# Performance work log

Hardware: AMD Instinct MI355X
Metric: run time of the kernel (lower is better)

The kernel has to match this reference:

```python
import jax, jax.numpy as jnp
import numpy as np

GAMMA = 2.0       # focal gamma (alpha=4.0 is unused in the original forward)
NC_LOOP = 20      # original loops cls in range(n_classes + 1) = 20 classes


def setup_inputs() -> dict:
    key = jax.random.key(0)
    k1, k2 = jax.random.split(key)
    B, C, H, W = 8, 20, 512, 512
    predictions = jax.random.normal(k1, (B, C, H, W), dtype=jnp.float32)
    labels = jax.random.randint(k2, (B, H, W), 0, C)
    # one-hot float target mask [B, C, H, W], as expected by BCE + argmax(dim=1)
    targets = jax.nn.one_hot(labels, C, axis=1, dtype=jnp.float32)
    return {"predictions": predictions, "targets": targets}


def reference(predictions, targets):
    p = jax.nn.softmax(predictions, axis=1)          # [B,C,H,W]
    bs = p.shape[0]
    ps = p.reshape(bs, -1)
    ts = targets.reshape(bs, -1)

    # BCELoss(reduction='none').mean(1); torch clamps log at -100
    log_p = jnp.clip(jnp.log(ps), -100.0)
    log_1mp = jnp.clip(jnp.log1p(-ps), -100.0)
    lseg = (-(ts * log_p + (1.0 - ts) * log_1mp)).mean(axis=1)  # [B]

    # focal loss: sum over class dim, mean over spatial dims
    fl = (-(targets * jnp.log(p + 1e-9)) * (1.0 - p) ** GAMMA).sum(axis=1)  # [B,H,W]
    fcl = fl.mean(axis=(1, 2))  # [B]

    # per-class IoU via per-batch class histograms (fused confusion-count pass)
    preds = jnp.argmax(p, axis=1).reshape(bs, -1)        # [B, HW]
    tgt = jnp.argmax(targets, axis=1).reshape(bs, -1)    # [B, HW]
    cnt_tgt = jax.vmap(lambda t: jnp.bincount(t, length=NC_LOOP))(tgt)     # [B,NC]
    cnt_pred = jax.vmap(lambda t: jnp.bincount(t, length=NC_LOOP))(preds)  # [B,NC]
    match = (preds == tgt).astype(jnp.float32)
    tp = jax.vmap(lambda t, w: jnp.bincount(t, weights=w, length=NC_LOOP))(tgt, match)
    fp = cnt_pred.astype(jnp.float32) - tp
    fn = cnt_tgt.astype(jnp.float32) - tp
    denom = tp + fp + fn
    # torch.nan_to_num(TP/denom): 0/0 -> 0
    iou_c = jnp.where(denom > 0, tp / jnp.maximum(denom, 1.0), 0.0)
    ious = iou_c.sum(axis=1)                                # [B]
    present = (cnt_tgt > 0).astype(jnp.float32).sum(axis=1)  # [B]
    iou = ious / present
    liou = 1.0 - iou

    return (lseg + liou + fcl).mean()
```

## Files before the change

kernel.cpp:

```cpp
#include <hip/hip_runtime.h>
#include <hip/hip_fp16.h>

#define NCLS 20
#define HW   (512 * 512)
#define TPB  256
#define PPT  2

#define ACC_STRIDE 64

typedef float v2f __attribute__((ext_vector_type(2)));

__global__ __launch_bounds__(TPB, 4) void seg_main(
    const float* __restrict__ pred,
    const float* __restrict__ tgt,
    unsigned* __restrict__ acc)
{
    __shared__ unsigned h_tgt[NCLS], h_pred[NCLS], h_tp[NCLS];
    __shared__ float red[8];

    const int tid = threadIdx.x;
    if (tid < NCLS) { h_tgt[tid] = 0u; h_pred[tid] = 0u; h_tp[tid] = 0u; }
    __syncthreads();

    const int b = blockIdx.y;
    const size_t pix = ((size_t)blockIdx.x * TPB + tid) * PPT;
    const float* pp = pred + (size_t)b * NCLS * HW + pix;
    const float* tp = tgt  + (size_t)b * NCLS * HW + pix;

    float S0 = 0.0f, S1 = 0.0f;
    float m0 = -1e30f, m1 = -1e30f;
    float xl0 = 0.0f, xl1 = 0.0f, el0 = 1.0f, el1 = 1.0f;
    int   pa0 = 0, pa1 = 0, lb0 = 0, lb1 = 0;
    __half2 eh0, eh1, eh2, eh3, eh4, eh5, eh6, eh7, eh8, eh9,
            eh10, eh11, eh12, eh13, eh14, eh15, eh16, eh17, eh18, eh19;

    v2f xv0, xv1, xv2, xv3, xv4, xv5, xv6, xv7, xv8, xv9,
        xv10, xv11, xv12, xv13, xv14, xv15, xv16, xv17, xv18, xv19;
    v2f tv0, tv1, tv2, tv3, tv4, tv5, tv6, tv7, tv8, tv9,
        tv10, tv11, tv12, tv13, tv14, tv15, tv16, tv17, tv18, tv19;

#define ISSUE4(c0, c1, c2, c3)                                              \
    asm volatile(                                                           \
        "global_load_dwordx2 %0, %8, off\n\t"                               \
        "global_load_dwordx2 %1, %9, off\n\t"                               \
        "global_load_dwordx2 %2, %10, off\n\t"                              \
        "global_load_dwordx2 %3, %11, off\n\t"                              \
        "global_load_dwordx2 %4, %12, off\n\t"                              \
        "global_load_dwordx2 %5, %13, off\n\t"                              \
        "global_load_dwordx2 %6, %14, off\n\t"                              \
        "global_load_dwordx2 %7, %15, off"                                  \
        : "=&v"(xv##c0), "=&v"(xv##c1), "=&v"(xv##c2), "=&v"(xv##c3),       \
          "=&v"(tv##c0), "=&v"(tv##c1), "=&v"(tv##c2), "=&v"(tv##c3)        \
        : "v"(pp + (size_t)(c0) * HW), "v"(pp + (size_t)(c1) * HW),         \
          "v"(pp + (size_t)(c2) * HW), "v"(pp + (size_t)(c3) * HW),         \
          "v"(tp + (size_t)(c0) * HW), "v"(tp + (size_t)(c1) * HW),         \
          "v"(tp + (size_t)(c2) * HW), "v"(tp + (size_t)(c3) * HW))

#define WAITV(N)                                              \
    asm volatile("s_waitcnt vmcnt(" #N ")" ::: "memory");     \
    __builtin_amdgcn_sched_barrier(0)

#define PROCC(c) {                                                          \
    const float xa = xv##c[0], xb = xv##c[1];                               \
    const float ea = __expf(xa), eb = __expf(xb);                           \
    const bool b0 = xa > m0, b1 = xb > m1;                                  \
    m0 = b0 ? xa : m0;  pa0 = b0 ? (c) : pa0;                               \
    m1 = b1 ? xb : m1;  pa1 = b1 ? (c) : pa1;                               \
    const bool i0 = tv##c[0] > 0.5f, i1 = tv##c[1] > 0.5f;                  \
    lb0 = i0 ? (c) : lb0;  xl0 = i0 ? xa : xl0;  el0 = i0 ? ea : el0;       \
    lb1 = i1 ? (c) : lb1;  xl1 = i1 ? xb : xl1;  el1 = i1 ? eb : el1;       \
    S0 += ea; S1 += eb;                                                     \
    eh##c = __floats2half2_rn(ea, eb); }

#define PROC4(c0, c1, c2, c3) PROCC(c0) PROCC(c1) PROCC(c2) PROCC(c3)

    ISSUE4(0, 1, 2, 3);
    ISSUE4(4, 5, 6, 7);
    ISSUE4(8, 9, 10, 11);
    WAITV(16);  ISSUE4(12, 13, 14, 15);  PROC4(0, 1, 2, 3);
    WAITV(16);  ISSUE4(16, 17, 18, 19);  PROC4(4, 5, 6, 7);
    WAITV(16);  PROC4(8, 9, 10, 11);
    WAITV(8);   PROC4(12, 13, 14, 15);
    WAITV(0);   PROC4(16, 17, 18, 19);

    float p10 = 1.0f, p11 = 1.0f, p20 = 1.0f, p21 = 1.0f;
#define BCEC(c) {                                                           \
    const float2 f = __half22float2(eh##c);                                 \
    const float ta = ((c) == lb0) ? 1.0f : fmaxf(S0 - f.x, 1e-30f);         \
    const float tb = ((c) == lb1) ? 1.0f : fmaxf(S1 - f.y, 1e-30f);         \
    if ((c) < 10) { p10 *= ta; p11 *= tb; } else { p20 *= ta; p21 *= tb; } }

    BCEC(0) BCEC(1) BCEC(2) BCEC(3) BCEC(4)
    BCEC(5) BCEC(6) BCEC(7) BCEC(8) BCEC(9)
    BCEC(10) BCEC(11) BCEC(12) BCEC(13) BCEC(14)
    BCEC(15) BCEC(16) BCEC(17) BCEC(18) BCEC(19)

    const float logS0 = __logf(S0), logS1 = __logf(S1);
    float tl = (20.0f * logS0 - xl0 - __logf(p10) - __logf(p20))
             + (20.0f * logS1 - xl1 - __logf(p11) - __logf(p21));
    const float q0 = 1.0f - el0 / S0, q1 = 1.0f - el1 / S1;
    float tf = -(xl0 - logS0) * q0 * q0 - (xl1 - logS1) * q1 * q1;

    atomicAdd(&h_tgt[lb0], 1u);
    atomicAdd(&h_tgt[lb1], 1u);
    atomicAdd(&h_pred[pa0], 1u);
    atomicAdd(&h_pred[pa1], 1u);
    if (pa0 == lb0) atomicAdd(&h_tp[lb0], 1u);
    if (pa1 == lb1) atomicAdd(&h_tp[lb1], 1u);

#pragma unroll
    for (int off = 32; off > 0; off >>= 1) {
        tl += __shfl_down(tl, off, 64);
        tf += __shfl_down(tf, off, 64);
    }
    const int wid = tid >> 6, lane = tid & 63;
    if (lane == 0) { red[wid] = tl; red[4 + wid] = tf; }
    __syncthreads();

    unsigned* ab = acc + (size_t)b * ACC_STRIDE;
    if (tid == 0) {
        const float a = red[0] + red[1] + red[2] + red[3];
        const float f = red[4] + red[5] + red[6] + red[7];
        atomicAdd(reinterpret_cast<float*>(ab + 0), a);
        atomicAdd(reinterpret_cast<float*>(ab + 1), f);
    }
    if (tid < NCLS) {
        atomicAdd(&ab[2  + tid], h_tgt[tid]);
        atomicAdd(&ab[22 + tid], h_pred[tid]);
        atomicAdd(&ab[42 + tid], h_tp[tid]);
    }
}

__global__ __launch_bounds__(256) void seg_final(
    const unsigned* __restrict__ acc, float* __restrict__ out, int nb)
{
    __shared__ float bl[8];
    const int tid = threadIdx.x;
    const int b = tid >> 5, c = tid & 31;

    float iou_c = 0.0f, pres = 0.0f;
    if (b < nb && c < NCLS) {
        const unsigned* ab = acc + (size_t)b * ACC_STRIDE;
        unsigned tg = ab[2 + c], pd = ab[22 + c], tpv = ab[42 + c];
        unsigned denom = tg + pd - tpv;
        if (tg > 0) pres = 1.0f;
        if (denom > 0) iou_c = (float)tpv / (float)denom;
    }
#pragma unroll
    for (int off = 16; off > 0; off >>= 1) {
        iou_c += __shfl_down(iou_c, off, 32);
        pres  += __shfl_down(pres,  off, 32);
    }
    if (c == 0 && b < nb) {
        const unsigned* ab = acc + (size_t)b * ACC_STRIDE;
        const float*    fs = reinterpret_cast<const float*>(ab);
        float lseg = fs[0] * (1.0f / ((float)NCLS * (float)HW));
        float fcl  = fs[1] * (1.0f / (float)HW);
        float iou  = (pres > 0.0f) ? (iou_c / pres) : 0.0f;
        bl[b] = lseg + (1.0f - iou) + fcl;
    }
    __syncthreads();
    if (tid == 0) {
        float t = 0.0f;
        for (int i = 0; i < nb; ++i) t += bl[i];
        out[0] = t / (float)nb;
    }
}

extern "C" void kernel_launch(void* const* d_in, const int* in_sizes, int n_in,
                              void* d_out, int out_size, void* d_ws, size_t ws_size,
                              hipStream_t stream)
{
    const float* pred = (const float*)d_in[0];
    const float* tgt  = (const float*)d_in[1];
    float* out = (float*)d_out;
    unsigned* acc = (unsigned*)d_ws;

    const int nb = in_sizes[0] / (NCLS * HW);

    hipMemsetAsync(acc, 0, (size_t)nb * ACC_STRIDE * sizeof(unsigned), stream);

    dim3 grid(HW / (TPB * PPT), nb);
    seg_main<<<grid, TPB, 0, stream>>>(pred, tgt, acc);
    seg_final<<<1, 256, 0, stream>>>(acc, out, nb);
}
```

Before: 92.05 us.

## Precompute byte labels and replace BCE log-product with power-series moments

Adds a separate pass that compacts the one-hot target tensor into one byte label per pixel, so the main kernel reads a byte instead of 20 floats per pixel for targets. The BCE sum over non-label classes is computed from a truncated Taylor series of log(1-p) using the first five power moments of exp(x), instead of storing half-precision exps and multiplying per-class terms. Pixels per thread go from 2 to 4, with dwordx4 loads. The label pass still reads the whole target tensor, so total traffic is not reduced, and the five-term series loses accuracy when any non-label class has a large probability.

```diff
diff --git a/kernel.cpp b/kernel.cpp
--- a/kernel.cpp
+++ b/kernel.cpp
@@ -1,18 +1,36 @@
 #include <hip/hip_runtime.h>
-#include <hip/hip_fp16.h>
 
 #define NCLS 20
 #define HW   (512 * 512)
 #define TPB  256
-#define PPT  2
+#define PPT  4
 
 #define ACC_STRIDE 64
 
-typedef float v2f __attribute__((ext_vector_type(2)));
+typedef float v4f __attribute__((ext_vector_type(4)));
+
+__global__ __launch_bounds__(256) void seg_label(
+    const float* __restrict__ tgt, unsigned char* __restrict__ lab,
+    unsigned nf4)
+{
+    const unsigned NTHR = 4096u * 256u;
+    for (unsigned e4 = blockIdx.x * 256u + threadIdx.x; e4 < nf4; e4 += NTHR) {
+        const float4 v = reinterpret_cast<const float4*>(tgt)[e4];
+        const unsigned f   = e4 * 4u;
+        const unsigned c   = (f >> 18) % NCLS;
+        const unsigned bb  = f / (NCLS * HW);
+        const unsigned pix = f & (HW - 1);
+        unsigned char* lp = lab + (size_t)bb * HW + pix;
+        if (v.x > 0.5f) lp[0] = (unsigned char)c;
+        if (v.y > 0.5f) lp[1] = (unsigned char)c;
+        if (v.z > 0.5f) lp[2] = (unsigned char)c;
+        if (v.w > 0.5f) lp[3] = (unsigned char)c;
+    }
+}
 
 __global__ __launch_bounds__(TPB, 4) void seg_main(
     const float* __restrict__ pred,
-    const float* __restrict__ tgt,
+    const unsigned char* __restrict__ lab,
     unsigned* __restrict__ acc)
 {
     __shared__ unsigned h_tgt[NCLS], h_pred[NCLS], h_tp[NCLS];
@@ -25,88 +43,84 @@
     const int b = blockIdx.y;
     const size_t pix = ((size_t)blockIdx.x * TPB + tid) * PPT;
     const float* pp = pred + (size_t)b * NCLS * HW + pix;
-    const float* tp = tgt  + (size_t)b * NCLS * HW + pix;
-
-    float S0 = 0.0f, S1 = 0.0f;
-    float m0 = -1e30f, m1 = -1e30f;
-    float xl0 = 0.0f, xl1 = 0.0f, el0 = 1.0f, el1 = 1.0f;
-    int   pa0 = 0, pa1 = 0, lb0 = 0, lb1 = 0;
-    __half2 eh0, eh1, eh2, eh3, eh4, eh5, eh6, eh7, eh8, eh9,
-            eh10, eh11, eh12, eh13, eh14, eh15, eh16, eh17, eh18, eh19;
-
-    v2f xv0, xv1, xv2, xv3, xv4, xv5, xv6, xv7, xv8, xv9,
+    const unsigned char* lpt = lab + (size_t)b * HW + pix;
+
+#define DECLPX(P) \
+    float M1_##P = 0.0f, M2_##P = 0.0f, M3_##P = 0.0f, M4_##P = 0.0f, \
+          M5_##P = 0.0f, mx_##P = -1e30f, xl_##P = 0.0f; \
+    int pa_##P = 0;
+    DECLPX(0) DECLPX(1) DECLPX(2) DECLPX(3)
+
+    v4f xv0, xv1, xv2, xv3, xv4, xv5, xv6, xv7, xv8, xv9,
         xv10, xv11, xv12, xv13, xv14, xv15, xv16, xv17, xv18, xv19;
-    v2f tv0, tv1, tv2, tv3, tv4, tv5, tv6, tv7, tv8, tv9,
-        tv10, tv11, tv12, tv13, tv14, tv15, tv16, tv17, tv18, tv19;
+    unsigned labu;
 
 #define ISSUE4(c0, c1, c2, c3)                                              \
     asm volatile(                                                           \
-        "global_load_dwordx2 %0, %8, off\n\t"                               \
-        "global_load_dwordx2 %1, %9, off\n\t"                               \
-        "global_load_dwordx2 %2, %10, off\n\t"                              \
-        "global_load_dwordx2 %3, %11, off\n\t"                              \
-        "global_load_dwordx2 %4, %12, off\n\t"                              \
-        "global_load_dwordx2 %5, %13, off\n\t"                              \
-        "global_load_dwordx2 %6, %14, off\n\t"                              \
-        "global_load_dwordx2 %7, %15, off"                                  \
-        : "=&v"(xv##c0), "=&v"(xv##c1), "=&v"(xv##c2), "=&v"(xv##c3),       \
-          "=&v"(tv##c0), "=&v"(tv##c1), "=&v"(tv##c2), "=&v"(tv##c3)        \
+        "global_load_dwordx4 %0, %4, off\n\t"                               \
+        "global_load_dwordx4 %1, %5, off\n\t"                               \
+        "global_load_dwordx4 %2, %6, off\n\t"                               \
+        "global_load_dwordx4 %3, %7, off"                                   \
+        : "=&v"(xv##c0), "=&v"(xv##c1), "=&v"(xv##c2), "=&v"(xv##c3)        \
         : "v"(pp + (size_t)(c0) * HW), "v"(pp + (size_t)(c1) * HW),         \
-          "v"(pp + (size_t)(c2) * HW), "v"(pp + (size_t)(c3) * HW),         \
-          "v"(tp + (size_t)(c0) * HW), "v"(tp + (size_t)(c1) * HW),         \
-          "v"(tp + (size_t)(c2) * HW), "v"(tp + (size_t)(c3) * HW))
+          "v"(pp + (size_t)(c2) * HW), "v"(pp + (size_t)(c3) * HW))
 
 #define WAITV(N)                                              \
     asm volatile("s_waitcnt vmcnt(" #N ")" ::: "memory");     \
     __builtin_amdgcn_sched_barrier(0)
 
-#define PROCC(c) {                                                          \
-    const float xa = xv##c[0], xb = xv##c[1];                               \
-    const float ea = __expf(xa), eb = __expf(xb);                           \
-    const bool b0 = xa > m0, b1 = xb > m1;                                  \
-    m0 = b0 ? xa : m0;  pa0 = b0 ? (c) : pa0;                               \
-    m1 = b1 ? xb : m1;  pa1 = b1 ? (c) : pa1;                               \
-    const bool i0 = tv##c[0] > 0.5f, i1 = tv##c[1] > 0.5f;                  \
-    lb0 = i0 ? (c) : lb0;  xl0 = i0 ? xa : xl0;  el0 = i0 ? ea : el0;       \
-    lb1 = i1 ? (c) : lb1;  xl1 = i1 ? xb : xl1;  el1 = i1 ? eb : el1;       \
-    S0 += ea; S1 += eb;                                                     \
-    eh##c = __floats2half2_rn(ea, eb); }
-
+#define PROC1(c, X, P) {                                                    \
+    const float x_ = (X);                                                   \
+    const float e_ = __expf(x_);                                            \
+    const float e2_ = e_ * e_, e3_ = e2_ * e_, e4_ = e2_ * e2_,             \
+                e5_ = e3_ * e2_;                                            \
+    M1_##P += e_; M2_##P += e2_; M3_##P += e3_; M4_##P += e4_;              \
+    M5_##P += e5_;                                                          \
+    const bool b_ = x_ > mx_##P;                                            \
+    mx_##P = b_ ? x_ : mx_##P;  pa_##P = b_ ? (c) : pa_##P;                 \
+    xl_##P = ((c) == lb##P) ? x_ : xl_##P; }
+
+#define PROCC(c) PROC1(c, xv##c.x, 0) PROC1(c, xv##c.y, 1) \
+                 PROC1(c, xv##c.z, 2) PROC1(c, xv##c.w, 3)
 #define PROC4(c0, c1, c2, c3) PROCC(c0) PROCC(c1) PROCC(c2) PROCC(c3)
 
+    asm volatile("global_load_dword %0, %1, off"
+                 : "=&v"(labu) : "v"(lpt));
     ISSUE4(0, 1, 2, 3);
     ISSUE4(4, 5, 6, 7);
     ISSUE4(8, 9, 10, 11);
-    WAITV(16);  ISSUE4(12, 13, 14, 15);  PROC4(0, 1, 2, 3);
-    WAITV(16);  ISSUE4(16, 17, 18, 19);  PROC4(4, 5, 6, 7);
-    WAITV(16);  PROC4(8, 9, 10, 11);
-    WAITV(8);   PROC4(12, 13, 14, 15);
+    WAITV(12);
+    const int lb0 = (int)(labu & 0xffu);
+    const int lb1 = (int)((labu >> 8) & 0xffu);
+    const int lb2 = (int)((labu >> 16) & 0xffu);
+    const int lb3 = (int)(labu >> 24);
+    WAITV(8);   PROC4(0, 1, 2, 3);   ISSUE4(12, 13, 14, 15);
+    WAITV(8);   PROC4(4, 5, 6, 7);   ISSUE4(16, 17, 18, 19);
+    WAITV(8);   PROC4(8, 9, 10, 11);
+    WAITV(4);   PROC4(12, 13, 14, 15);
     WAITV(0);   PROC4(16, 17, 18, 19);
 
-    float p10 = 1.0f, p11 = 1.0f, p20 = 1.0f, p21 = 1.0f;
-#define BCEC(c) {                                                           \
-    const float2 f = __half22float2(eh##c);                                 \
-    const float ta = ((c) == lb0) ? 1.0f : fmaxf(S0 - f.x, 1e-30f);         \
-    const float tb = ((c) == lb1) ? 1.0f : fmaxf(S1 - f.y, 1e-30f);         \
-    if ((c) < 10) { p10 *= ta; p11 *= tb; } else { p20 *= ta; p21 *= tb; } }
-
-    BCEC(0) BCEC(1) BCEC(2) BCEC(3) BCEC(4)
-    BCEC(5) BCEC(6) BCEC(7) BCEC(8) BCEC(9)
-    BCEC(10) BCEC(11) BCEC(12) BCEC(13) BCEC(14)
-    BCEC(15) BCEC(16) BCEC(17) BCEC(18) BCEC(19)
-
-    const float logS0 = __logf(S0), logS1 = __logf(S1);
-    float tl = (20.0f * logS0 - xl0 - __logf(p10) - __logf(p20))
-             + (20.0f * logS1 - xl1 - __logf(p11) - __logf(p21));
-    const float q0 = 1.0f - el0 / S0, q1 = 1.0f - el1 / S1;
-    float tf = -(xl0 - logS0) * q0 * q0 - (xl1 - logS1) * q1 * q1;
-
-    atomicAdd(&h_tgt[lb0], 1u);
-    atomicAdd(&h_tgt[lb1], 1u);
-    atomicAdd(&h_pred[pa0], 1u);
-    atomicAdd(&h_pred[pa1], 1u);
-    if (pa0 == lb0) atomicAdd(&h_tp[lb0], 1u);
-    if (pa1 == lb1) atomicAdd(&h_tp[lb1], 1u);
+    float tl = 0.0f, tf = 0.0f;
+#define FINPX(P) {                                                          \
+    const float S_ = M1_##P;                                                \
+    const float is_ = 1.0f / S_;                                            \
+    const float is2_ = is_ * is_;                                           \
+    const float logS_ = __logf(S_);                                         \
+    const float ser_ = 1.0f + 0.5f * M2_##P * is2_                          \
+                     + 0.33333333f * M3_##P * is2_ * is_                    \
+                     + 0.25f * M4_##P * is2_ * is2_                         \
+                     + 0.2f * M5_##P * is2_ * is2_ * is_;                   \
+    const float loglab_ = xl_##P - logS_;                                   \
+    const float plab_ = __expf(xl_##P) * is_;                               \
+    const float l1m_ = __logf(fmaxf(1.0f - plab_, 1e-37f));                 \
+    tl += ser_ + l1m_ - loglab_;                                            \
+    const float om_ = 1.0f - plab_;                                         \
+    tf -= loglab_ * om_ * om_;                                              \
+    atomicAdd(&h_tgt[lb##P], 1u);                                           \
+    atomicAdd(&h_pred[pa_##P], 1u);                                         \
+    if (pa_##P == lb##P) atomicAdd(&h_tp[lb##P], 1u); }
+
+    FINPX(0) FINPX(1) FINPX(2) FINPX(3)
 
 #pragma unroll
     for (int off = 32; off > 0; off >>= 1) {
@@ -175,12 +189,16 @@
     const float* tgt  = (const float*)d_in[1];
     float* out = (float*)d_out;
     unsigned* acc = (unsigned*)d_ws;
+    unsigned char* labels = (unsigned char*)d_ws + 4096;
 
     const int nb = in_sizes[0] / (NCLS * HW);
+    const unsigned nf4 = (unsigned)(in_sizes[1] / 4);
 
     hipMemsetAsync(acc, 0, (size_t)nb * ACC_STRIDE * sizeof(unsigned), stream);
 
+    seg_label<<<4096, 256, 0, stream>>>(tgt, labels, nf4);
+
     dim3 grid(HW / (TPB * PPT), nb);
-    seg_main<<<grid, TPB, 0, stream>>>(pred, tgt, acc);
+    seg_main<<<grid, TPB, 0, stream>>>(pred, labels, acc);
     seg_final<<<1, 256, 0, stream>>>(acc, out, nb);
 }
```

Result: no change. 90.37 us (-1.8%).
